# Optimization experiments

Hardware: AMD Instinct MI355X
Metric: run time of the kernel (lower is better)

The kernel has to match this reference:

```python
import jax, jax.numpy as jnp
import numpy as np

N = 100000
E = 1600000
D = 64
BETA = 1.0


def setup_inputs() -> dict:
    key = jax.random.key(0)
    ks = jax.random.split(key, 6)
    x = jax.random.normal(ks[0], (N, D), dtype=jnp.float32)
    edge_index = jax.random.randint(ks[1], (2, E), 0, N, dtype=jnp.int64)
    s = 1.0 / np.sqrt(D)
    Wm = jax.random.uniform(ks[2], (D, D), jnp.float32, -s, s)
    bm = jax.random.uniform(ks[3], (D,), jnp.float32, -s, s)
    Wr = jax.random.uniform(ks[4], (D, D), jnp.float32, -s, s)
    br = jax.random.uniform(ks[5], (D,), jnp.float32, -s, s)
    return {"x": x, "edge_index": edge_index, "Wm": Wm, "bm": bm, "Wr": Wr, "br": br}


def reference(x, edge_index, Wm, bm, Wr, br):
    row, col = edge_index[0], edge_index[1]
    # gather source features and apply message linear: [E, D]
    messages = x[row] @ Wm + bm
    scores = BETA * messages.mean(axis=-1)  # [E]
    # edge softmax over incoming edges of each destination node (col)
    seg_max = jax.ops.segment_max(scores, col, num_segments=N)  # [N]
    ex = jnp.exp(scores - seg_max[col])  # [E]
    seg_sum = jax.ops.segment_sum(ex, col, num_segments=N)  # [N]
    weights = ex / seg_sum[col]  # [E]
    # weighted scatter-add back to destinations
    out = jax.ops.segment_sum(messages * weights[:, None], col, num_segments=N)
    return out + (x @ Wr + br)
```

## Files before the change

kernel.cpp:

```cpp
#include <hip/hip_runtime.h>
#include <math.h>

#define N_NODES 100000
#define DIM 64
#define N_EDGES 1600000

#define NBF 782
#define BK_NODES 128
#define CAP 3072

#define SC_CHUNK 8192
#define SC_BLOCKS ((N_EDGES + SC_CHUNK - 1) / SC_CHUNK)

#define GEMM_BLOCKS ((N_NODES / 16 + 15) / 16)
#define PH_BLOCKS (SC_BLOCKS + GEMM_BLOCKS)

typedef _Float16 half8 __attribute__((ext_vector_type(8)));
typedef _Float16 half4 __attribute__((ext_vector_type(4)));
typedef float f32x4 __attribute__((ext_vector_type(4)));

__global__ __launch_bounds__(1024) void k_phase(
        const float* __restrict__ x,
        const float* __restrict__ Wm, const float* __restrict__ bm,
        const float* __restrict__ Wr, const float* __restrict__ br,
        const int* __restrict__ row, const int* __restrict__ col,
        int* __restrict__ cursor, unsigned int* __restrict__ pairs,
        _Float16* __restrict__ Mh, float* __restrict__ es,
        float* __restrict__ out) {
    __shared__ int cnt[NBF];
    __shared__ int base_l[NBF];
    __shared__ int base_g[NBF];
    __shared__ int wsum[16];
    __shared__ unsigned int stage[SC_CHUNK];
    __shared__ unsigned short stage_bk[SC_CHUNK];

    const int t = threadIdx.x;
    const int lane = t & 63;
    const int wid = t >> 6;

    if (blockIdx.x < SC_BLOCKS) {
        const int start = blockIdx.x * SC_CHUNK;
        const int mEnd = min(N_EDGES, start + SC_CHUNK);

        for (int i = t; i < NBF; i += 1024) cnt[i] = 0;
        __syncthreads();

        int rr[8], cc[8], lr[8];
#pragma unroll
        for (int k = 0; k < 8; ++k) {
            const int idx = start + k * 1024 + t;
            if (idx < mEnd) {
                cc[k] = col[idx];
                rr[k] = row[idx];
                lr[k] = atomicAdd(&cnt[cc[k] >> 7], 1);
            }
        }
        __syncthreads();

        const int v = (t < NBF) ? cnt[t] : 0;
        int inc = v;
#pragma unroll
        for (int o = 1; o < 64; o <<= 1) {
            const int u = __shfl_up(inc, o, 64);
            if (lane >= o) inc += u;
        }
        if (lane == 63) wsum[wid] = inc;
        __syncthreads();
        if (wid == 0) {
            const int wv = (lane < 16) ? wsum[lane] : 0;
            int winc = wv;
#pragma unroll
            for (int o = 1; o < 16; o <<= 1) {
                const int u = __shfl_up(winc, o, 64);
                if (lane >= o) winc += u;
            }
            if (lane < 16) wsum[lane] = winc - wv;
        }
        __syncthreads();
        if (t < NBF) {
            base_l[t] = inc - v + wsum[wid];
            if (v > 0) base_g[t] = atomicAdd(&cursor[t], v);
        }
        __syncthreads();

#pragma unroll
        for (int k = 0; k < 8; ++k) {
            const int idx = start + k * 1024 + t;
            if (idx < mEnd) {
                const int bk = cc[k] >> 7;
                const int slot = base_l[bk] + lr[k];
                stage[slot] = ((unsigned int)rr[k] << 7) | (unsigned int)(cc[k] & 127);
                stage_bk[slot] = (unsigned short)bk;
            }
        }
        __syncthreads();

        const int m = mEnd - start;
        for (int i = t; i < m; i += 1024) {
            const int bk = stage_bk[i];
            const int gslot = base_g[bk] + (i - base_l[bk]);
            if (gslot < CAP) pairs[(size_t)bk * CAP + gslot] = stage[i];
        }
        return;
    }

    const int wave = (blockIdx.x - SC_BLOCKS) * 16 + wid;
    if (wave >= N_NODES / 16) return;
    const int quad = lane >> 4;
    const int l15 = lane & 15;
    const int row0 = wave * 16;

    half8 bfrag[8][2];
#pragma unroll
    for (int ct = 0; ct < 8; ++ct) {
        const float* W = (ct < 4) ? Wm : Wr;
        const int c = (ct & 3) * 16 + l15;
#pragma unroll
        for (int kc = 0; kc < 2; ++kc) {
            half8 f;
#pragma unroll
            for (int j = 0; j < 8; ++j)
                f[j] = (_Float16)W[(kc * 32 + quad * 8 + j) * DIM + c];
            bfrag[ct][kc] = f;
        }
    }

    half8 afrag[2];
#pragma unroll
    for (int kc = 0; kc < 2; ++kc) {
        const float* xp = x + (size_t)(row0 + l15) * DIM + kc * 32 + quad * 8;
        const float4 x0 = *(const float4*)xp;
        const float4 x1 = *(const float4*)(xp + 4);
        half8 f;
        f[0] = (_Float16)x0.x; f[1] = (_Float16)x0.y;
        f[2] = (_Float16)x0.z; f[3] = (_Float16)x0.w;
        f[4] = (_Float16)x1.x; f[5] = (_Float16)x1.y;
        f[6] = (_Float16)x1.z; f[7] = (_Float16)x1.w;
        afrag[kc] = f;
    }

    f32x4 acc[8];
#pragma unroll
    for (int ct = 0; ct < 8; ++ct) {
        f32x4 a = {0.f, 0.f, 0.f, 0.f};
        a = __builtin_amdgcn_mfma_f32_16x16x32_f16(afrag[0], bfrag[ct][0], a, 0, 0, 0);
        a = __builtin_amdgcn_mfma_f32_16x16x32_f16(afrag[1], bfrag[ct][1], a, 0, 0, 0);
        acc[ct] = a;
    }

    float rsum[4] = {0.f, 0.f, 0.f, 0.f};
#pragma unroll
    for (int ct = 0; ct < 8; ++ct) {
        const float bias = (ct < 4) ? bm[(ct & 3) * 16 + l15]
                                    : br[(ct & 3) * 16 + l15];
#pragma unroll
        for (int r = 0; r < 4; ++r) {
            const float v = acc[ct][r] + bias;
            const size_t idx = (size_t)(row0 + quad * 4 + r) * DIM + (ct & 3) * 16 + l15;
            if (ct < 4) {
                Mh[idx] = (_Float16)v;
                rsum[r] += v;
            } else {
                out[idx] = v;
            }
        }
    }
#pragma unroll
    for (int o = 1; o <= 8; o <<= 1) {
#pragma unroll
        for (int r = 0; r < 4; ++r) rsum[r] += __shfl_xor(rsum[r], o, 64);
    }
    if (l15 == 0) {
#pragma unroll
        for (int r = 0; r < 4; ++r)
            es[row0 + quad * 4 + r] = __expf(rsum[r] * (1.0f / DIM));
    }
}

__global__ __launch_bounds__(512) void k_bucket_gather(
        const unsigned int* __restrict__ pairs, const int* __restrict__ cursor,
        const float* __restrict__ es, const half4* __restrict__ Mh4,
        float4* __restrict__ out4) {
    __shared__ unsigned int sorted[CAP];
    __shared__ int cnt[BK_NODES];
    __shared__ int off[BK_NODES];
    const int b = blockIdx.x;
    const int t = threadIdx.x;
    const int m = min(cursor[b], CAP);
    const size_t base = (size_t)b * CAP;

    if (t < BK_NODES) cnt[t] = 0;
    __syncthreads();

    unsigned int pk[6];
    int rk[6];
#pragma unroll
    for (int k = 0; k < 6; ++k) {
        const int i = k * 512 + t;
        if (i < m) {
            pk[k] = pairs[base + i];
            rk[k] = atomicAdd(&cnt[pk[k] & 127u], 1);
        }
    }
    __syncthreads();

    int v = 0;
    if (t < BK_NODES) {
        v = cnt[t];
        off[t] = v;
    }
    __syncthreads();
    for (int o = 1; o < BK_NODES; o <<= 1) {
        int add = 0;
        if (t < BK_NODES && t >= o) add = off[t - o];
        __syncthreads();
        if (t < BK_NODES) off[t] += add;
        __syncthreads();
    }
    if (t < BK_NODES) off[t] -= v;
    __syncthreads();

#pragma unroll
    for (int k = 0; k < 6; ++k) {
        const int i = k * 512 + t;
        if (i < m) sorted[off[pk[k] & 127u] + rk[k]] = pk[k];
    }
    __syncthreads();

    const int g = t >> 4;
    const int gl = t & 15;
    for (int c = g; c < BK_NODES; c += 32) {
        const int node = b * BK_NODES + c;
        if (node >= N_NODES) break;
        const int s0i = off[c];
        const int len = cnt[c];
        if (len == 0) continue;

        float a0x = 0.f, a0y = 0.f, a0z = 0.f, a0w = 0.f, l0 = 0.f;
        float a1x = 0.f, a1y = 0.f, a1z = 0.f, a1w = 0.f, l1 = 0.f;
        int j = 0;
        for (; j + 1 < len; j += 2) {
            const int s0 = (int)(sorted[s0i + j] >> 7);
            const int s1 = (int)(sorted[s0i + j + 1] >> 7);
            const float w0 = es[s0];
            const float w1 = es[s1];
            const half4 m0 = Mh4[(size_t)s0 * 16 + gl];
            const half4 m1 = Mh4[(size_t)s1 * 16 + gl];
            l0 += w0; l1 += w1;
            a0x = fmaf(w0, (float)m0[0], a0x); a0y = fmaf(w0, (float)m0[1], a0y);
            a0z = fmaf(w0, (float)m0[2], a0z); a0w = fmaf(w0, (float)m0[3], a0w);
            a1x = fmaf(w1, (float)m1[0], a1x); a1y = fmaf(w1, (float)m1[1], a1y);
            a1z = fmaf(w1, (float)m1[2], a1z); a1w = fmaf(w1, (float)m1[3], a1w);
        }
        if (j < len) {
            const int s0 = (int)(sorted[s0i + j] >> 7);
            const float w0 = es[s0];
            const half4 m0 = Mh4[(size_t)s0 * 16 + gl];
            l0 += w0;
            a0x = fmaf(w0, (float)m0[0], a0x); a0y = fmaf(w0, (float)m0[1], a0y);
            a0z = fmaf(w0, (float)m0[2], a0z); a0w = fmaf(w0, (float)m0[3], a0w);
        }
        const float inv = 1.0f / (l0 + l1);
        float4 r = out4[(size_t)node * 16 + gl];
        r.x = fmaf(a0x + a1x, inv, r.x);
        r.y = fmaf(a0y + a1y, inv, r.y);
        r.z = fmaf(a0z + a1z, inv, r.z);
        r.w = fmaf(a0w + a1w, inv, r.w);
        out4[(size_t)node * 16 + gl] = r;
    }
}

extern "C" void kernel_launch(void* const* d_in, const int* in_sizes, int n_in,
                              void* d_out, int out_size, void* d_ws, size_t ws_size,
                              hipStream_t stream) {
    const float* x  = (const float*)d_in[0];
    const int*   ei = (const int*)d_in[1];
    const float* Wm = (const float*)d_in[2];
    const float* bm = (const float*)d_in[3];
    const float* Wr = (const float*)d_in[4];
    const float* br = (const float*)d_in[5];
    float* out = (float*)d_out;
    const int* row = ei;
    const int* col = ei + N_EDGES;

    char* ws = (char*)d_ws;
    _Float16* Mh    = (_Float16*)ws;     ws += (size_t)N_NODES * DIM * sizeof(_Float16);
    float* es       = (float*)ws;        ws += (size_t)N_NODES * sizeof(float);
    int* cursor     = (int*)ws;          ws += (size_t)1024 * sizeof(int);
    unsigned int* pairs = (unsigned int*)ws; ws += (size_t)NBF * CAP * sizeof(unsigned int);

    hipMemsetAsync(cursor, 0, NBF * sizeof(int), stream);

    k_phase<<<PH_BLOCKS, 1024, 0, stream>>>(x, Wm, bm, Wr, br, row, col,
                                            cursor, pairs, Mh, es, out);
    k_bucket_gather<<<NBF, 512, 0, stream>>>(pairs, cursor, es,
                                             (const half4*)Mh, (float4*)out);
}
```

Measured before the change: 157.3 us.

## Stage weights in LDS, use nontemporal memory ops, widen bucket-gather blocks

GEMM blocks now cooperatively convert Wm/Wr to fp16 into shared memory (a padded transposed layout reusing the stage buffer), so each wave loads B fragments as vector LDS reads instead of strided scalar global loads. Streaming loads and stores of edges, pairs, x and out are marked nontemporal to reduce cache pollution. The bucket-gather kernel moves to 1024 threads, handling two nodes per 16-lane group, and swaps the barrier-heavy shared-memory scan for a wave shuffle scan. The larger block may lower occupancy, and nontemporal hints on out could hurt, since the gather kernel reads out back.

```diff
diff --git a/kernel.cpp b/kernel.cpp
--- a/kernel.cpp
+++ b/kernel.cpp
@@ -18,6 +18,9 @@
 typedef _Float16 half8 __attribute__((ext_vector_type(8)));
 typedef _Float16 half4 __attribute__((ext_vector_type(4)));
 typedef float f32x4 __attribute__((ext_vector_type(4)));
+
+#define WL_CSTride 72
+#define WL_MStride (64 * WL_CSTride)
 
 __global__ __launch_bounds__(1024) void k_phase(
         const float* __restrict__ x,
@@ -50,8 +53,8 @@
         for (int k = 0; k < 8; ++k) {
             const int idx = start + k * 1024 + t;
             if (idx < mEnd) {
-                cc[k] = col[idx];
-                rr[k] = row[idx];
+                cc[k] = __builtin_nontemporal_load(&col[idx]);
+                rr[k] = __builtin_nontemporal_load(&row[idx]);
                 lr[k] = atomicAdd(&cnt[cc[k] >> 7], 1);
             }
         }
@@ -99,10 +102,21 @@
         for (int i = t; i < m; i += 1024) {
             const int bk = stage_bk[i];
             const int gslot = base_g[bk] + (i - base_l[bk]);
-            if (gslot < CAP) pairs[(size_t)bk * CAP + gslot] = stage[i];
+            if (gslot < CAP)
+                __builtin_nontemporal_store(stage[i], &pairs[(size_t)bk * CAP + gslot]);
         }
         return;
     }
+
+    _Float16* Wl = (_Float16*)stage;
+    for (int i = t; i < 2 * 64 * 64; i += 1024) {
+        const int m2 = i >> 12;
+        const int k  = (i >> 6) & 63;
+        const int c  = i & 63;
+        const float* W = m2 ? Wr : Wm;
+        Wl[m2 * WL_MStride + c * WL_CSTride + k] = (_Float16)W[k * 64 + c];
+    }
+    __syncthreads();
 
     const int wave = (blockIdx.x - SC_BLOCKS) * 16 + wid;
     if (wave >= N_NODES / 16) return;
@@ -113,15 +127,12 @@
     half8 bfrag[8][2];
 #pragma unroll
     for (int ct = 0; ct < 8; ++ct) {
-        const float* W = (ct < 4) ? Wm : Wr;
         const int c = (ct & 3) * 16 + l15;
+        const int m2 = ct >> 2;
 #pragma unroll
         for (int kc = 0; kc < 2; ++kc) {
-            half8 f;
-#pragma unroll
-            for (int j = 0; j < 8; ++j)
-                f[j] = (_Float16)W[(kc * 32 + quad * 8 + j) * DIM + c];
-            bfrag[ct][kc] = f;
+            bfrag[ct][kc] = *(const half8*)
+                &Wl[m2 * WL_MStride + c * WL_CSTride + kc * 32 + quad * 8];
         }
     }
 
@@ -129,13 +140,13 @@
 #pragma unroll
     for (int kc = 0; kc < 2; ++kc) {
         const float* xp = x + (size_t)(row0 + l15) * DIM + kc * 32 + quad * 8;
-        const float4 x0 = *(const float4*)xp;
-        const float4 x1 = *(const float4*)(xp + 4);
+        const f32x4 x0 = __builtin_nontemporal_load((const f32x4*)xp);
+        const f32x4 x1 = __builtin_nontemporal_load((const f32x4*)(xp + 4));
         half8 f;
-        f[0] = (_Float16)x0.x; f[1] = (_Float16)x0.y;
-        f[2] = (_Float16)x0.z; f[3] = (_Float16)x0.w;
-        f[4] = (_Float16)x1.x; f[5] = (_Float16)x1.y;
-        f[6] = (_Float16)x1.z; f[7] = (_Float16)x1.w;
+        f[0] = (_Float16)x0[0]; f[1] = (_Float16)x0[1];
+        f[2] = (_Float16)x0[2]; f[3] = (_Float16)x0[3];
+        f[4] = (_Float16)x1[0]; f[5] = (_Float16)x1[1];
+        f[6] = (_Float16)x1[2]; f[7] = (_Float16)x1[3];
         afrag[kc] = f;
     }
 
@@ -161,7 +172,7 @@
                 Mh[idx] = (_Float16)v;
                 rsum[r] += v;
             } else {
-                out[idx] = v;
+                __builtin_nontemporal_store(v, &out[idx]);
             }
         }
     }
@@ -177,61 +188,68 @@
     }
 }
 
-__global__ __launch_bounds__(512) void k_bucket_gather(
+__global__ __launch_bounds__(1024) void k_bucket_gather(
         const unsigned int* __restrict__ pairs, const int* __restrict__ cursor,
         const float* __restrict__ es, const half4* __restrict__ Mh4,
-        float4* __restrict__ out4) {
+        float* __restrict__ out) {
     __shared__ unsigned int sorted[CAP];
     __shared__ int cnt[BK_NODES];
     __shared__ int off[BK_NODES];
+    __shared__ int wtot[2];
     const int b = blockIdx.x;
     const int t = threadIdx.x;
+    const int lane = t & 63;
+    const int wid = t >> 6;
     const int m = min(cursor[b], CAP);
     const size_t base = (size_t)b * CAP;
 
     if (t < BK_NODES) cnt[t] = 0;
     __syncthreads();
 
-    unsigned int pk[6];
-    int rk[6];
-#pragma unroll
-    for (int k = 0; k < 6; ++k) {
-        const int i = k * 512 + t;
+    unsigned int pk[3];
+    int rk[3];
+#pragma unroll
+    for (int k = 0; k < 3; ++k) {
+        const int i = k * 1024 + t;
         if (i < m) {
-            pk[k] = pairs[base + i];
+            pk[k] = __builtin_nontemporal_load(&pairs[base + i]);
             rk[k] = atomicAdd(&cnt[pk[k] & 127u], 1);
         }
     }
     __syncthreads();
 
-    int v = 0;
+    int v = 0, inc = 0;
     if (t < BK_NODES) {
         v = cnt[t];
-        off[t] = v;
-    }
-    __syncthreads();
-    for (int o = 1; o < BK_NODES; o <<= 1) {
-        int add = 0;
-        if (t < BK_NODES && t >= o) add = off[t - o];
-        __syncthreads();
-        if (t < BK_NODES) off[t] += add;
-        __syncthreads();
-    }
-    if (t < BK_NODES) off[t] -= v;
-    __syncthreads();
-
-#pragma unroll
-    for (int k = 0; k < 6; ++k) {
-        const int i = k * 512 + t;
+        inc = v;
+#pragma unroll
+        for (int o = 1; o < 64; o <<= 1) {
+            const int u = __shfl_up(inc, o, 64);
+            if (lane >= o) inc += u;
+        }
+        if (lane == 63) wtot[wid] = inc;
+    }
+    __syncthreads();
+    if (t < BK_NODES) {
+        const int add = (wid == 1) ? wtot[0] : 0;
+        off[t] = inc - v + add;
+    }
+    __syncthreads();
+
+#pragma unroll
+    for (int k = 0; k < 3; ++k) {
+        const int i = k * 1024 + t;
         if (i < m) sorted[off[pk[k] & 127u] + rk[k]] = pk[k];
     }
     __syncthreads();
 
     const int g = t >> 4;
     const int gl = t & 15;
-    for (int c = g; c < BK_NODES; c += 32) {
+#pragma unroll
+    for (int half = 0; half < 2; ++half) {
+        const int c = g + half * 64;
         const int node = b * BK_NODES + c;
-        if (node >= N_NODES) break;
+        if (node >= N_NODES) continue;
         const int s0i = off[c];
         const int len = cnt[c];
         if (len == 0) continue;
@@ -261,12 +279,13 @@
             a0z = fmaf(w0, (float)m0[2], a0z); a0w = fmaf(w0, (float)m0[3], a0w);
         }
         const float inv = 1.0f / (l0 + l1);
-        float4 r = out4[(size_t)node * 16 + gl];
-        r.x = fmaf(a0x + a1x, inv, r.x);
-        r.y = fmaf(a0y + a1y, inv, r.y);
-        r.z = fmaf(a0z + a1z, inv, r.z);
-        r.w = fmaf(a0w + a1w, inv, r.w);
-        out4[(size_t)node * 16 + gl] = r;
+        f32x4* op = (f32x4*)(out + (size_t)node * DIM + gl * 4);
+        f32x4 r = __builtin_nontemporal_load(op);
+        r[0] = fmaf(a0x + a1x, inv, r[0]);
+        r[1] = fmaf(a0y + a1y, inv, r[1]);
+        r[2] = fmaf(a0z + a1z, inv, r[2]);
+        r[3] = fmaf(a0w + a1w, inv, r[3]);
+        __builtin_nontemporal_store(r, op);
     }
 }
 
@@ -293,6 +312,6 @@
 
     k_phase<<<PH_BLOCKS, 1024, 0, stream>>>(x, Wm, bm, Wr, br, row, col,
                                             cursor, pairs, Mh, es, out);
-    k_bucket_gather<<<NBF, 512, 0, stream>>>(pairs, cursor, es,
-                                             (const half4*)Mh, (float4*)out);
+    k_bucket_gather<<<NBF, 1024, 0, stream>>>(pairs, cursor, es,
+                                              (const half4*)Mh, out);
 }
```

Measured after the change: 161.4 us. +2.6%, slower.
